# Kernel tuning notes

Measured on AMD Instinct MI355X. Metric: run time of the kernel, lower is better.

The kernel has to match this reference:

```python
import jax, jax.numpy as jnp
import numpy as np

N = 1_000_000  # total_voxels
V = 128        # volume_size


def setup_inputs() -> dict:
    key = jax.random.key(0)
    ks = jax.random.split(key, 10)
    inds = jax.random.randint(ks[0], (N, 3), 0, V, dtype=jnp.int32)
    reference_values = jax.random.normal(ks[1], (1, N), dtype=jnp.float32)
    # SIREN-ish init scales: ~1/sqrt(fan_in) keeps sin() inputs O(1); tiny final
    # layer scale keeps delta_coords sub-voxel (as training would).
    W0 = jax.random.normal(ks[2], (3 * N, 8), dtype=jnp.float32) / np.float32(np.sqrt(3 * N))
    W1 = jax.random.normal(ks[3], (8, 8), dtype=jnp.float32) / np.float32(np.sqrt(8))
    W2 = jax.random.normal(ks[4], (8, 8), dtype=jnp.float32) / np.float32(np.sqrt(8))
    W3 = jax.random.normal(ks[5], (8, 8), dtype=jnp.float32) / np.float32(np.sqrt(8))
    W4 = jax.random.normal(ks[6], (8, 8), dtype=jnp.float32) / np.float32(np.sqrt(8))
    W5 = jax.random.normal(ks[7], (8, 4 * N), dtype=jnp.float32) * np.float32(0.01 / np.sqrt(8))
    z8 = jnp.zeros((8,), jnp.float32)
    return {
        "inds": inds, "reference_values": reference_values,
        "W0": W0, "b0": z8, "W1": W1, "b1": z8, "W2": W2, "b2": z8,
        "W3": W3, "b3": z8, "W4": W4, "b4": z8,
        "W5": W5, "b5": jnp.zeros((4 * N,), jnp.float32),
        "volume_size": V,
    }


def reference(inds, reference_values, W0, b0, W1, b1, W2, b2, W3, b3, W4, b4,
              W5, b5, volume_size):
    n = inds.shape[0]
    factor = 0.5 * volume_size
    # normalized coords buffer: stack (z,y,x) columns -> (1, N, 3) in [-1, 1)
    coords_n = (jnp.stack([inds[:, 2], inds[:, 1], inds[:, 0]], axis=1)[None]
                .astype(jnp.float32) - factor) / factor
    # tiny SIREN MLP on the flattened coord vector (1, 3N)
    x = jnp.sin(coords_n.reshape(1, -1) @ W0 + b0)
    for W, b in ((W1, b1), (W2, b2), (W3, b3), (W4, b4)):
        x = x + jnp.sin(x @ W + b)
    x = (x @ W5 + b5).reshape(1, n, 4)          # (1, N, 4)
    delta_coords, delta_values = x[..., :3], x[..., 3]
    values = jax.nn.relu(reference_values + delta_values)      # (1, N)
    coords = factor * (coords_n + delta_coords) + factor       # voxel-space, (1, N, 3)
    # trilinear 8-corner splat
    bposf = jnp.floor(coords)
    bposi = bposf.astype(jnp.int32)                             # (1, N, 3)
    f = coords - bposf
    fx, fy, fz = f[..., 0], f[..., 1], f[..., 2]
    gx, gy, gz = 1.0 - fx, 1.0 - fy, 1.0 - fz
    bamp = jnp.concatenate([
        values * gx * gy * gz, values * fx * gy * gz,
        values * gx * fy * gz, values * gx * gy * fz,
        values * gx * fy * fz, values * fx * gy * fz,
        values * fx * fy * gz, values * fx * fy * fz,
    ], axis=1)                                                  # (1, 8N)
    offs = jnp.array([[0, 0, 0], [1, 0, 0], [0, 1, 0], [0, 0, 1],
                      [0, 1, 1], [1, 0, 1], [1, 1, 0], [1, 1, 1]], jnp.int32)
    bpos = jnp.concatenate([bposi + o for o in offs], axis=1)   # (1, 8N, 3)
    vol0 = jnp.zeros((values.shape[0], volume_size, volume_size, volume_size),
                     jnp.float32)

    def scatter(vol, p, a):  # out-of-bounds corners are dropped (jax default)
        return vol.at[p[:, 2], p[:, 1], p[:, 0]].add(a)

    return jax.vmap(scatter, in_axes=(0, 0, 0))(vol0, bpos, bamp)
```

## Files before the change

### kernel.cpp

```cpp
#include <hip/hip_runtime.h>
#include <hip/hip_bf16.h>

constexpr int V = 128;
constexpr int NTILES = 512;
constexpr int TD = 17;
constexpr int TSIZE = TD * TD * TD;
constexpr int TPAD = 5120;
constexpr int NS = 16;
constexpr int CAPS = 256;
constexpr int CNT_INTS = NS * NTILES * 16;

__global__ __launch_bounds__(256) void k_reduce_w0(
    const int* __restrict__ inds, const float* __restrict__ W0,
    float* __restrict__ partials, float4* __restrict__ vol4,
    int4* __restrict__ cnt4, int threeN) {
  int g = blockIdx.x * 256 + threadIdx.x;
  vol4[g] = make_float4(0.f, 0.f, 0.f, 0.f);
  if (cnt4 && g < CNT_INTS / 4) cnt4[g] = make_int4(0, 0, 0, 0);

  float acc[8];
#pragma unroll
  for (int k = 0; k < 8; ++k) acc[k] = 0.f;

  int stride = gridDim.x * blockDim.x;
  for (int j = g; j < threeN; j += stride) {
    int c = j % 3;
    float cval = ((float)inds[j + 2 - 2 * c] - 64.0f) * 0.015625f;
    const float4* w = (const float4*)(W0 + (size_t)j * 8);
    float4 a = w[0];
    float4 b = w[1];
    acc[0] += cval * a.x; acc[1] += cval * a.y;
    acc[2] += cval * a.z; acc[3] += cval * a.w;
    acc[4] += cval * b.x; acc[5] += cval * b.y;
    acc[6] += cval * b.z; acc[7] += cval * b.w;
  }

#pragma unroll
  for (int off = 32; off > 0; off >>= 1) {
#pragma unroll
    for (int k = 0; k < 8; ++k) acc[k] += __shfl_down(acc[k], off);
  }

  __shared__ float red[4][8];
  int wave = threadIdx.x >> 6;
  int lane = threadIdx.x & 63;
  if (lane == 0) {
#pragma unroll
    for (int k = 0; k < 8; ++k) red[wave][k] = acc[k];
  }
  __syncthreads();
  if (threadIdx.x < 8) {
    int k = threadIdx.x;
    partials[(size_t)blockIdx.x * 8 + k] = red[0][k] + red[1][k] + red[2][k] + red[3][k];
  }
}

__global__ __launch_bounds__(256) void k_mlp(
    const float* __restrict__ partials, int nb,
    const float* __restrict__ b0,
    const float* __restrict__ W1, const float* __restrict__ b1,
    const float* __restrict__ W2, const float* __restrict__ b2,
    const float* __restrict__ W3, const float* __restrict__ b3,
    const float* __restrict__ W4, const float* __restrict__ b4,
    float* __restrict__ x8_out) {
  __shared__ float red[256];
  __shared__ float accv[8];
  int tid = threadIdx.x;
  int k = tid & 7;
  float s = 0.f;
  for (int b = tid >> 3; b < nb; b += 32) s += partials[(size_t)b * 8 + k];
  red[tid] = s;
  __syncthreads();
  if (tid < 8) {
    float t = 0.f;
    for (int j = tid; j < 256; j += 8) t += red[j];
    accv[tid] = t;
  }
  __syncthreads();
  if (tid == 0) {
    float x[8];
#pragma unroll
    for (int kk = 0; kk < 8; ++kk) x[kk] = sinf(accv[kk] + b0[kk]);
    const float* Ws[4] = {W1, W2, W3, W4};
    const float* bs[4] = {b1, b2, b3, b4};
    for (int l = 0; l < 4; ++l) {
      float t[8];
#pragma unroll
      for (int kk = 0; kk < 8; ++kk) {
        float ss = bs[l][kk];
#pragma unroll
        for (int j = 0; j < 8; ++j) ss += x[j] * Ws[l][j * 8 + kk];
        t[kk] = ss;
      }
#pragma unroll
      for (int kk = 0; kk < 8; ++kk) x[kk] += sinf(t[kk]);
    }
#pragma unroll
    for (int kk = 0; kk < 8; ++kk) x8_out[kk] = x[kk];
  }
}

__device__ inline int tile_of(float cx, float cy, float cz) {
  int bx = (int)floorf(cx), by = (int)floorf(cy), bz = (int)floorf(cz);
  int tx = min(max(bx, 0), V - 1) >> 4;
  int ty = min(max(by, 0), V - 1) >> 4;
  int tz = min(max(bz, 0), V - 1) >> 4;
  return (tz << 6) | (ty << 3) | tx;
}

__device__ inline void scatter_direct(float* vol, float cx, float cy, float cz,
                                      float value) {
  float bxf = floorf(cx), byf = floorf(cy), bzf = floorf(cz);
  int bx = (int)bxf, by = (int)byf, bz = (int)bzf;
  float fx = cx - bxf, fy = cy - byf, fz = cz - bzf;
  float gx = 1.f - fx, gy = 1.f - fy, gz = 1.f - fz;
#pragma unroll
  for (int dz = 0; dz < 2; ++dz)
#pragma unroll
    for (int dy = 0; dy < 2; ++dy)
#pragma unroll
      for (int dx = 0; dx < 2; ++dx) {
        float w = value * (dx ? fx : gx) * (dy ? fy : gy) * (dz ? fz : gz);
        int px = bx + dx, py = by + dy, pz = bz + dz;
        if (px < 0) px += V;
        if (py < 0) py += V;
        if (pz < 0) pz += V;
        if ((unsigned)px < (unsigned)V && (unsigned)py < (unsigned)V &&
            (unsigned)pz < (unsigned)V)
          atomicAdd(vol + ((size_t)pz * V * V + (size_t)py * V + px), w);
      }
}

__global__ __launch_bounds__(256) void k_decode_scatter(
    const int* __restrict__ inds, const float* __restrict__ refv,
    const float* __restrict__ W5, const float* __restrict__ b5,
    const float* __restrict__ x8_buf, float4* __restrict__ srt,
    int* __restrict__ cnt, float* __restrict__ vol, int N) {
  __shared__ float x8[8];
  if (threadIdx.x < 8) x8[threadIdx.x] = x8_buf[threadIdx.x];
  __syncthreads();

  int i = blockIdx.x * 256 + threadIdx.x;
  if (i >= N) return;

  const size_t fourN = (size_t)4 * N;
  float4 o = *(const float4*)(b5 + (size_t)4 * i);
  float out0 = o.x, out1 = o.y, out2 = o.z, out3 = o.w;
#pragma unroll
  for (int k = 0; k < 8; ++k) {
    float xv = x8[k];
    float4 w = *(const float4*)(W5 + (size_t)k * fourN + (size_t)4 * i);
    out0 += xv * w.x; out1 += xv * w.y; out2 += xv * w.z; out3 += xv * w.w;
  }
  float value = refv[i] + out3;
  value = value > 0.f ? value : 0.f;
  if (value <= 0.f) return;

  int i0 = inds[3 * i], i1 = inds[3 * i + 1], i2 = inds[3 * i + 2];
  float cx = (((float)i2 - 64.0f) * 0.015625f + out0) * 64.0f + 64.0f;
  float cy = (((float)i1 - 64.0f) * 0.015625f + out1) * 64.0f + 64.0f;
  float cz = (((float)i0 - 64.0f) * 0.015625f + out2) * 64.0f + 64.0f;

  int t = tile_of(cx, cy, cz);
  int s = blockIdx.x & (NS - 1);
  int slot = s * NTILES + t;
  int pos = atomicAdd(&cnt[slot * 16], 1);
  if (pos < CAPS) {
    srt[(size_t)slot * CAPS + pos] = make_float4(cx, cy, cz, value);
  } else {
    scatter_direct(vol, cx, cy, cz, value);
  }
}

__global__ __launch_bounds__(256) void k_tile(
    const float4* __restrict__ srt, const int* __restrict__ cnt,
    float* __restrict__ priv, float* __restrict__ vol) {
  __shared__ float tl[TSIZE];
  int t = blockIdx.x;
  int ox = (t & 7) << 4, oy = ((t >> 3) & 7) << 4, oz = (t >> 6) << 4;
  for (int j = threadIdx.x; j < TSIZE; j += 256) tl[j] = 0.f;
  __syncthreads();

  for (int s = 0; s < NS; ++s) {
    int slot = s * NTILES + t;
    int c = min(cnt[slot * 16], CAPS);
    const float4* base = srt + (size_t)slot * CAPS;
    for (int i = threadIdx.x; i < c; i += 256) {
      float4 r = base[i];
      float bxf = floorf(r.x), byf = floorf(r.y), bzf = floorf(r.z);
      int bx = (int)bxf, by = (int)byf, bz = (int)bzf;
      float fx = r.x - bxf, fy = r.y - byf, fz = r.z - bzf;
      float gx = 1.f - fx, gy = 1.f - fy, gz = 1.f - fz;
      float value = r.w;

#pragma unroll
      for (int dz = 0; dz < 2; ++dz) {
#pragma unroll
        for (int dy = 0; dy < 2; ++dy) {
#pragma unroll
          for (int dx = 0; dx < 2; ++dx) {
            float w = value * (dx ? fx : gx) * (dy ? fy : gy) * (dz ? fz : gz);
            int px = bx + dx, py = by + dy, pz = bz + dz;
            if (px < 0) px += V;
            if (py < 0) py += V;
            if (pz < 0) pz += V;
            if (px >= V || py >= V || pz >= V) continue;
            int lx = px - ox, ly = py - oy, lz = pz - oz;
            if ((unsigned)lx < (unsigned)TD && (unsigned)ly < (unsigned)TD &&
                (unsigned)lz < (unsigned)TD) {
              atomicAdd(&tl[lz * (TD * TD) + ly * TD + lx], w);
            } else {
              atomicAdd(vol + ((size_t)pz * V * V + (size_t)py * V + px), w);
            }
          }
        }
      }
    }
  }
  __syncthreads();
  for (int j = threadIdx.x; j < TSIZE; j += 256) priv[(size_t)t * TPAD + j] = tl[j];
}

__global__ __launch_bounds__(256) void k_gather(const float* __restrict__ priv,
                                                float* __restrict__ vol) {
  int idx = blockIdx.x * 256 + threadIdx.x;
  int x = idx & 127, y = (idx >> 7) & 127, z = idx >> 14;
  float s = vol[idx];
  int txs[2] = {x >> 4, (x >> 4) - 1}, lxs[2] = {x & 15, 16};
  int tys[2] = {y >> 4, (y >> 4) - 1}, lys[2] = {y & 15, 16};
  int tzs[2] = {z >> 4, (z >> 4) - 1}, lzs[2] = {z & 15, 16};
  int nx = ((x & 15) == 0 && x > 0) ? 2 : 1;
  int ny = ((y & 15) == 0 && y > 0) ? 2 : 1;
  int nz = ((z & 15) == 0 && z > 0) ? 2 : 1;
  for (int iz = 0; iz < nz; ++iz)
    for (int iy = 0; iy < ny; ++iy)
      for (int ix = 0; ix < nx; ++ix) {
        int t = (tzs[iz] << 6) | (tys[iy] << 3) | txs[ix];
        s += priv[(size_t)t * TPAD + lzs[iz] * (TD * TD) + lys[iy] * TD + lxs[ix]];
      }
  vol[idx] = s;
}

__global__ __launch_bounds__(256) void k_scatter(
    const int* __restrict__ inds, const float* __restrict__ refv,
    const float* __restrict__ W5, const float* __restrict__ b5,
    const float* __restrict__ x8_buf, float* __restrict__ vol, int N) {
  __shared__ float x8[8];
  if (threadIdx.x < 8) x8[threadIdx.x] = x8_buf[threadIdx.x];
  __syncthreads();
  int i = blockIdx.x * blockDim.x + threadIdx.x;
  if (i >= N) return;
  const size_t fourN = (size_t)4 * N;
  float4 o = *(const float4*)(b5 + (size_t)4 * i);
  float out0 = o.x, out1 = o.y, out2 = o.z, out3 = o.w;
#pragma unroll
  for (int k = 0; k < 8; ++k) {
    float xv = x8[k];
    float4 w = *(const float4*)(W5 + (size_t)k * fourN + (size_t)4 * i);
    out0 += xv * w.x; out1 += xv * w.y; out2 += xv * w.z; out3 += xv * w.w;
  }
  float value = refv[i] + out3;
  value = value > 0.f ? value : 0.f;
  int i0 = inds[3 * i], i1 = inds[3 * i + 1], i2 = inds[3 * i + 2];
  float cx = (((float)i2 - 64.0f) * 0.015625f + out0) * 64.0f + 64.0f;
  float cy = (((float)i1 - 64.0f) * 0.015625f + out1) * 64.0f + 64.0f;
  float cz = (((float)i0 - 64.0f) * 0.015625f + out2) * 64.0f + 64.0f;
  scatter_direct(vol, cx, cy, cz, value);
}

extern "C" void kernel_launch(void* const* d_in, const int* in_sizes, int n_in,
                              void* d_out, int out_size, void* d_ws, size_t ws_size,
                              hipStream_t stream) {
  const int*   inds = (const int*)d_in[0];
  const float* refv = (const float*)d_in[1];
  const float* W0   = (const float*)d_in[2];
  const float* b0   = (const float*)d_in[3];
  const float* W1   = (const float*)d_in[4];
  const float* b1   = (const float*)d_in[5];
  const float* W2   = (const float*)d_in[6];
  const float* b2   = (const float*)d_in[7];
  const float* W3   = (const float*)d_in[8];
  const float* b3   = (const float*)d_in[9];
  const float* W4   = (const float*)d_in[10];
  const float* b4   = (const float*)d_in[11];
  const float* W5   = (const float*)d_in[12];
  const float* b5   = (const float*)d_in[13];

  int N = in_sizes[0] / 3;
  float* vol = (float*)d_out;
  char* w = (char*)d_ws;

  const int NB_R = 2048;
  float*  x8       = (float*)(w + 0);
  float*  partials = (float*)(w + 256);
  int*    cnt      = (int*)(w + 131072);
  float4* srt      = (float4*)(w + 1048576);
  float*  priv     = (float*)(srt + (size_t)NS * NTILES * CAPS);

  size_t needed = (size_t)1048576 + (size_t)NS * NTILES * CAPS * 16 +
                  (size_t)NTILES * TPAD * 4;

  if (ws_size >= needed) {
    k_reduce_w0<<<NB_R, 256, 0, stream>>>(inds, W0, partials, (float4*)vol,
                                          (int4*)cnt, 3 * N);
    k_mlp<<<1, 256, 0, stream>>>(partials, NB_R, b0, W1, b1, W2, b2, W3, b3, W4, b4, x8);
    k_decode_scatter<<<(N + 255) / 256, 256, 0, stream>>>(inds, refv, W5, b5, x8,
                                                          srt, cnt, vol, N);
    k_tile<<<NTILES, 256, 0, stream>>>(srt, cnt, priv, vol);
    k_gather<<<(V * V * V) / 256, 256, 0, stream>>>(priv, vol);
  } else {
    hipMemsetAsync(d_out, 0, (size_t)out_size * sizeof(float), stream);
    k_reduce_w0<<<NB_R, 256, 0, stream>>>(inds, W0, partials, (float4*)vol,
                                          (int4*)nullptr, 3 * N);
    k_mlp<<<1, 256, 0, stream>>>(partials, NB_R, b0, W1, b1, W2, b2, W3, b3, W4, b4, x8);
    k_scatter<<<(N + 255) / 256, 256, 0, stream>>>(inds, refv, W5, b5, x8, vol, N);
  }
}
```

Measured before the change: 361.3 us.

## Fuse tile flush into global volume with atomics and use nontemporal weight loads

Removes the private tile buffer and the separate gather kernel. Each tile block now atomically adds its nonzero shared-memory voxels straight into the output volume. The tile kernel also flattens the per-stream loop into one combined index range, so threads stay busy across all streams. Streaming weight loads in the W0 reduction and the W5 decode switch to nontemporal loads to reduce cache pollution. The cost is extra global atomics at tile borders and on every nonzero voxel.

After: 341.4 us. -5.5%, faster.

```diff
diff --git a/kernel.cpp b/kernel.cpp
--- a/kernel.cpp
+++ b/kernel.cpp
@@ -5,10 +5,14 @@
 constexpr int NTILES = 512;
 constexpr int TD = 17;
 constexpr int TSIZE = TD * TD * TD;
-constexpr int TPAD = 5120;
 constexpr int NS = 16;
 constexpr int CAPS = 256;
 constexpr int CNT_INTS = NS * NTILES * 16;
+
+typedef float __attribute__((ext_vector_type(4))) f4_t;
+__device__ __forceinline__ f4_t ldnt(const float* p) {
+  return __builtin_nontemporal_load((const f4_t*)p);
+}
 
 __global__ __launch_bounds__(256) void k_reduce_w0(
     const int* __restrict__ inds, const float* __restrict__ W0,
@@ -26,9 +30,9 @@
   for (int j = g; j < threeN; j += stride) {
     int c = j % 3;
     float cval = ((float)inds[j + 2 - 2 * c] - 64.0f) * 0.015625f;
-    const float4* w = (const float4*)(W0 + (size_t)j * 8);
-    float4 a = w[0];
-    float4 b = w[1];
+    const float* w = W0 + (size_t)j * 8;
+    f4_t a = ldnt(w);
+    f4_t b = ldnt(w + 4);
     acc[0] += cval * a.x; acc[1] += cval * a.y;
     acc[2] += cval * a.z; acc[3] += cval * a.w;
     acc[4] += cval * b.x; acc[5] += cval * b.y;
@@ -144,12 +148,12 @@
   if (i >= N) return;
 
   const size_t fourN = (size_t)4 * N;
-  float4 o = *(const float4*)(b5 + (size_t)4 * i);
+  f4_t o = ldnt(b5 + (size_t)4 * i);
   float out0 = o.x, out1 = o.y, out2 = o.z, out3 = o.w;
 #pragma unroll
   for (int k = 0; k < 8; ++k) {
     float xv = x8[k];
-    float4 w = *(const float4*)(W5 + (size_t)k * fourN + (size_t)4 * i);
+    f4_t w = ldnt(W5 + (size_t)k * fourN + (size_t)4 * i);
     out0 += xv * w.x; out1 += xv * w.y; out2 += xv * w.z; out3 += xv * w.w;
   }
   float value = refv[i] + out3;
@@ -172,73 +176,78 @@
   }
 }
 
-__global__ __launch_bounds__(256) void k_tile(
+__global__ __launch_bounds__(256) void k_tile_fused(
     const float4* __restrict__ srt, const int* __restrict__ cnt,
-    float* __restrict__ priv, float* __restrict__ vol) {
+    float* __restrict__ vol) {
   __shared__ float tl[TSIZE];
+  __shared__ int scnt_sh[NS];
   int t = blockIdx.x;
   int ox = (t & 7) << 4, oy = ((t >> 3) & 7) << 4, oz = (t >> 6) << 4;
   for (int j = threadIdx.x; j < TSIZE; j += 256) tl[j] = 0.f;
-  __syncthreads();
-
-  for (int s = 0; s < NS; ++s) {
-    int slot = s * NTILES + t;
-    int c = min(cnt[slot * 16], CAPS);
-    const float4* base = srt + (size_t)slot * CAPS;
-    for (int i = threadIdx.x; i < c; i += 256) {
-      float4 r = base[i];
-      float bxf = floorf(r.x), byf = floorf(r.y), bzf = floorf(r.z);
-      int bx = (int)bxf, by = (int)byf, bz = (int)bzf;
-      float fx = r.x - bxf, fy = r.y - byf, fz = r.z - bzf;
-      float gx = 1.f - fx, gy = 1.f - fy, gz = 1.f - fz;
-      float value = r.w;
-
-#pragma unroll
-      for (int dz = 0; dz < 2; ++dz) {
-#pragma unroll
-        for (int dy = 0; dy < 2; ++dy) {
-#pragma unroll
-          for (int dx = 0; dx < 2; ++dx) {
-            float w = value * (dx ? fx : gx) * (dy ? fy : gy) * (dz ? fz : gz);
-            int px = bx + dx, py = by + dy, pz = bz + dz;
-            if (px < 0) px += V;
-            if (py < 0) py += V;
-            if (pz < 0) pz += V;
-            if (px >= V || py >= V || pz >= V) continue;
-            int lx = px - ox, ly = py - oy, lz = pz - oz;
-            if ((unsigned)lx < (unsigned)TD && (unsigned)ly < (unsigned)TD &&
-                (unsigned)lz < (unsigned)TD) {
-              atomicAdd(&tl[lz * (TD * TD) + ly * TD + lx], w);
-            } else {
-              atomicAdd(vol + ((size_t)pz * V * V + (size_t)py * V + px), w);
-            }
+  if (threadIdx.x < NS) {
+    int slot = threadIdx.x * NTILES + t;
+    scnt_sh[threadIdx.x] = min(cnt[slot * 16], CAPS);
+  }
+  __syncthreads();
+
+  int cb[NS];
+  int total = 0;
+#pragma unroll
+  for (int k = 0; k < NS; ++k) { cb[k] = total; total += scnt_sh[k]; }
+
+  for (int i = threadIdx.x; i < total; i += 256) {
+    int s = 0, base = 0;
+#pragma unroll
+    for (int k = 1; k < NS; ++k) {
+      bool ge = (i >= cb[k]);
+      s = ge ? k : s;
+      base = ge ? cb[k] : base;
+    }
+    float4 r = srt[((size_t)(s * NTILES + t)) * CAPS + (i - base)];
+
+    float bxf = floorf(r.x), byf = floorf(r.y), bzf = floorf(r.z);
+    int bx = (int)bxf, by = (int)byf, bz = (int)bzf;
+    float fx = r.x - bxf, fy = r.y - byf, fz = r.z - bzf;
+    float gx = 1.f - fx, gy = 1.f - fy, gz = 1.f - fz;
+    float value = r.w;
+
+#pragma unroll
+    for (int dz = 0; dz < 2; ++dz) {
+#pragma unroll
+      for (int dy = 0; dy < 2; ++dy) {
+#pragma unroll
+        for (int dx = 0; dx < 2; ++dx) {
+          float w = value * (dx ? fx : gx) * (dy ? fy : gy) * (dz ? fz : gz);
+          int px = bx + dx, py = by + dy, pz = bz + dz;
+          if (px < 0) px += V;
+          if (py < 0) py += V;
+          if (pz < 0) pz += V;
+          if (px >= V || py >= V || pz >= V) continue;
+          int lx = px - ox, ly = py - oy, lz = pz - oz;
+          if ((unsigned)lx < (unsigned)TD && (unsigned)ly < (unsigned)TD &&
+              (unsigned)lz < (unsigned)TD) {
+            atomicAdd(&tl[lz * (TD * TD) + ly * TD + lx], w);
+          } else {
+            atomicAdd(vol + ((size_t)pz * V * V + (size_t)py * V + px), w);
           }
         }
       }
     }
   }
   __syncthreads();
-  for (int j = threadIdx.x; j < TSIZE; j += 256) priv[(size_t)t * TPAD + j] = tl[j];
-}
-
-__global__ __launch_bounds__(256) void k_gather(const float* __restrict__ priv,
-                                                float* __restrict__ vol) {
-  int idx = blockIdx.x * 256 + threadIdx.x;
-  int x = idx & 127, y = (idx >> 7) & 127, z = idx >> 14;
-  float s = vol[idx];
-  int txs[2] = {x >> 4, (x >> 4) - 1}, lxs[2] = {x & 15, 16};
-  int tys[2] = {y >> 4, (y >> 4) - 1}, lys[2] = {y & 15, 16};
-  int tzs[2] = {z >> 4, (z >> 4) - 1}, lzs[2] = {z & 15, 16};
-  int nx = ((x & 15) == 0 && x > 0) ? 2 : 1;
-  int ny = ((y & 15) == 0 && y > 0) ? 2 : 1;
-  int nz = ((z & 15) == 0 && z > 0) ? 2 : 1;
-  for (int iz = 0; iz < nz; ++iz)
-    for (int iy = 0; iy < ny; ++iy)
-      for (int ix = 0; ix < nx; ++ix) {
-        int t = (tzs[iz] << 6) | (tys[iy] << 3) | txs[ix];
-        s += priv[(size_t)t * TPAD + lzs[iz] * (TD * TD) + lys[iy] * TD + lxs[ix]];
-      }
-  vol[idx] = s;
+
+  for (int j = threadIdx.x; j < TSIZE; j += 256) {
+    float v = tl[j];
+    if (v != 0.f) {
+      int lz = j / (TD * TD);
+      int rem = j - lz * (TD * TD);
+      int ly = rem / TD;
+      int lx = rem - ly * TD;
+      int px = ox + lx, py = oy + ly, pz = oz + lz;
+      if (px < V && py < V && pz < V)
+        atomicAdd(vol + ((size_t)pz * V * V + (size_t)py * V + px), v);
+    }
+  }
 }
 
 __global__ __launch_bounds__(256) void k_scatter(
@@ -295,10 +304,8 @@
   float*  partials = (float*)(w + 256);
   int*    cnt      = (int*)(w + 131072);
   float4* srt      = (float4*)(w + 1048576);
-  float*  priv     = (float*)(srt + (size_t)NS * NTILES * CAPS);
-
-  size_t needed = (size_t)1048576 + (size_t)NS * NTILES * CAPS * 16 +
-                  (size_t)NTILES * TPAD * 4;
+
+  size_t needed = (size_t)1048576 + (size_t)NS * NTILES * CAPS * 16;
 
   if (ws_size >= needed) {
     k_reduce_w0<<<NB_R, 256, 0, stream>>>(inds, W0, partials, (float4*)vol,
@@ -306,8 +313,7 @@
     k_mlp<<<1, 256, 0, stream>>>(partials, NB_R, b0, W1, b1, W2, b2, W3, b3, W4, b4, x8);
     k_decode_scatter<<<(N + 255) / 256, 256, 0, stream>>>(inds, refv, W5, b5, x8,
                                                           srt, cnt, vol, N);
-    k_tile<<<NTILES, 256, 0, stream>>>(srt, cnt, priv, vol);
-    k_gather<<<(V * V * V) / 256, 256, 0, stream>>>(priv, vol);
+    k_tile_fused<<<NTILES, 256, 0, stream>>>(srt, cnt, vol);
   } else {
     hipMemsetAsync(d_out, 0, (size_t)out_size * sizeof(float), stream);
     k_reduce_w0<<<NB_R, 256, 0, stream>>>(inds, W0, partials, (float4*)vol,
```
